# Optimization experiments

Hardware: AMD Instinct MI355X
Metric: run time of the kernel (lower is better)

Reference implementation:

```python
import jax, jax.numpy as jnp
import numpy as np

N = 200000          # nodes
E = 12_800_000      # edges (avg degree 64)
C = 4               # conv_out_channels == node_features
H = 32              # lstm_out_channels


def setup_inputs() -> dict:
    key = jax.random.key(0)
    ks = jax.random.split(key, 16)
    inv_c = 1.0 / np.sqrt(C)
    inv_h = 1.0 / np.sqrt(H)
    return {
        "x": jax.random.normal(ks[0], (N, C), jnp.float32),
        "edge_index": jax.random.randint(ks[1], (2, E), 0, N, dtype=jnp.int64),
        "edge_weight": jax.random.uniform(ks[2], (E,), jnp.float32),
        "h_0": 0.1 * jax.random.normal(ks[3], (1, N, H), jnp.float32),
        "c_0": 0.1 * jax.random.normal(ks[4], (1, N, H), jnp.float32),
        # GatedGraphConv (num_layers=1): weight[0] of shape [C, C]
        "conv_weight": inv_c * jax.random.normal(ks[5], (C, C), jnp.float32),
        # GRUCell(C, C) params (PyTorch layout: [3C, C], gate order r,z,n)
        "gru_w_ih": inv_c * jax.random.normal(ks[6], (3 * C, C), jnp.float32),
        "gru_w_hh": inv_c * jax.random.normal(ks[7], (3 * C, C), jnp.float32),
        "gru_b_ih": inv_c * jax.random.normal(ks[8], (3 * C,), jnp.float32),
        "gru_b_hh": inv_c * jax.random.normal(ks[9], (3 * C,), jnp.float32),
        # LSTM(C, H, 1 layer) params (PyTorch layout: [4H, *], gate order i,f,g,o)
        "lstm_w_ih": inv_h * jax.random.normal(ks[10], (4 * H, C), jnp.float32),
        "lstm_w_hh": inv_h * jax.random.normal(ks[11], (4 * H, H), jnp.float32),
        "lstm_b_ih": inv_h * jax.random.normal(ks[12], (4 * H,), jnp.float32),
        "lstm_b_hh": inv_h * jax.random.normal(ks[13], (4 * H,), jnp.float32),
        # Linear(32, 1)
        "lin_w": inv_h * jax.random.normal(ks[14], (1, H), jnp.float32),
        "lin_b": inv_h * jax.random.normal(ks[15], (1,), jnp.float32),
    }


def reference(x, edge_index, edge_weight, h_0, c_0,
              conv_weight, gru_w_ih, gru_w_hh, gru_b_ih, gru_b_hh,
              lstm_w_ih, lstm_w_hh, lstm_b_ih, lstm_b_hh, lin_w, lin_b):
    n = x.shape[0]
    src, dst = edge_index[0], edge_index[1]  # source j -> target i

    # ---- GatedGraphConv, 1 layer (in_dim == out_channels, no padding) ----
    m = x @ conv_weight                                   # [N, C]
    msg = m[src] * edge_weight[:, None]                   # [E, C] gather
    summed = jax.ops.segment_sum(msg, dst, num_segments=n)
    cnt = jax.ops.segment_sum(jnp.ones((msg.shape[0],), msg.dtype), dst,
                              num_segments=n)
    agg = summed / jnp.maximum(cnt, 1.0)[:, None]         # mean aggr (empty -> 0)

    # GRUCell(agg, x): r,z,n gate order
    gi = agg @ gru_w_ih.T + gru_b_ih
    gh = x @ gru_w_hh.T + gru_b_hh
    i_r, i_z, i_n = jnp.split(gi, 3, axis=1)
    h_r, h_z, h_n = jnp.split(gh, 3, axis=1)
    r = jax.nn.sigmoid(i_r + h_r)
    z = jax.nn.sigmoid(i_z + h_z)
    nn_ = jnp.tanh(i_n + r * h_n)
    h_conv = (1.0 - z) * nn_ + z * x                      # [N, C]

    # ---- LSTM: seq_len=1, batch=N, 1 layer; gate order i,f,g,o ----
    h_prev, c_prev = h_0[0], c_0[0]                       # [N, H]
    gates = h_conv @ lstm_w_ih.T + lstm_b_ih + h_prev @ lstm_w_hh.T + lstm_b_hh
    ig, fg, gg, og = jnp.split(gates, 4, axis=1)
    ig, fg, og = jax.nn.sigmoid(ig), jax.nn.sigmoid(fg), jax.nn.sigmoid(og)
    gg = jnp.tanh(gg)
    c_new = fg * c_prev + ig * gg
    h_new = og * jnp.tanh(c_new)                          # [N, H]

    # ---- relu + linear head ----
    out = jax.nn.relu(h_new) @ lin_w.T + lin_b            # [N, 1]
    return out, h_new[None], c_new[None]
```

## Files before the change

### kernel.cpp

```cpp
#include <hip/hip_runtime.h>
#include <math.h>

#define B_SHIFT 8
#define BMASK   255
#define CHUNK   16384
#define NTHR    256

static __device__ __forceinline__ float sigf(float x) {
  return 1.0f / (1.0f + __expf(-x));
}
static __device__ __forceinline__ float tanhfast(float x) {
  return 2.0f / (1.0f + __expf(-2.0f * x)) - 1.0f;
}

__global__ void conv_m_kernel(const float* __restrict__ x,
                              const float* __restrict__ w,
                              float* __restrict__ m, int n) {
  int i = blockIdx.x * blockDim.x + threadIdx.x;
  if (i >= n) return;
  float4 xv = reinterpret_cast<const float4*>(x)[i];
  float4 mv;
  mv.x = xv.x * w[0] + xv.y * w[4] + xv.z * w[8]  + xv.w * w[12];
  mv.y = xv.x * w[1] + xv.y * w[5] + xv.z * w[9]  + xv.w * w[13];
  mv.z = xv.x * w[2] + xv.y * w[6] + xv.z * w[10] + xv.w * w[14];
  mv.w = xv.x * w[3] + xv.y * w[7] + xv.z * w[11] + xv.w * w[15];
  reinterpret_cast<float4*>(m)[i] = mv;
}


__global__ __launch_bounds__(NTHR) void hist_kernel(const int* __restrict__ dst,
                                                    int E, int B,
                                                    int* __restrict__ gCnt) {
  __shared__ int h[1024];
  for (int b = threadIdx.x; b < B; b += NTHR) h[b] = 0;
  __syncthreads();
  const int4* d4 = reinterpret_cast<const int4*>(dst);
  int i4base = (int)(((long long)blockIdx.x * CHUNK) >> 2);
  int lim4 = E >> 2;
#pragma unroll
  for (int j = 0; j < 16; ++j) {
    int i4 = i4base + j * NTHR + threadIdx.x;
    if (i4 < lim4) {
      int4 d = d4[i4];
      atomicAdd(&h[d.x >> B_SHIFT], 1);
      atomicAdd(&h[d.y >> B_SHIFT], 1);
      atomicAdd(&h[d.z >> B_SHIFT], 1);
      atomicAdd(&h[d.w >> B_SHIFT], 1);
    }
  }
  if (blockIdx.x == 0 && threadIdx.x == 0) {
    for (int e = E & ~3; e < E; ++e) atomicAdd(&h[dst[e] >> B_SHIFT], 1);
  }
  __syncthreads();
  for (int b = threadIdx.x; b < B; b += NTHR) {
    int c = h[b];
    if (c) atomicAdd(&gCnt[b], c);
  }
}

__global__ void scan_kernel(const int* __restrict__ gCnt, int B,
                            int* __restrict__ start, int* __restrict__ cursor) {
  __shared__ int s[1024];
  int t = threadIdx.x;
  int v = (t < B) ? gCnt[t] : 0;
  s[t] = v;
  __syncthreads();
  for (int off = 1; off < 1024; off <<= 1) {
    int u = (t >= off) ? s[t - off] : 0;
    __syncthreads();
    s[t] += u;
    __syncthreads();
  }
  if (t < B) {
    int excl = (t == 0) ? 0 : s[t - 1];
    start[t] = excl;
    cursor[t] = excl;
  }
  if (t == 0) start[B] = s[1023];
}

__global__ __launch_bounds__(NTHR) void bin_kernel(const int* __restrict__ ei,
                                                   const float* __restrict__ ew,
                                                   int E, int B,
                                                   int* __restrict__ cursor,
                                                   int2* __restrict__ binned) {
  __shared__ int h[1024];
  for (int b = threadIdx.x; b < B; b += NTHR) h[b] = 0;
  __syncthreads();
  const int* dst = ei + E;
  const int4* d4 = reinterpret_cast<const int4*>(dst);
  const int4* s4 = reinterpret_cast<const int4*>(ei);
  const float4* w4 = reinterpret_cast<const float4*>(ew);
  int i4base = (int)(((long long)blockIdx.x * CHUNK) >> 2);
  int lim4 = E >> 2;
#pragma unroll
  for (int j = 0; j < 16; ++j) {
    int i4 = i4base + j * NTHR + threadIdx.x;
    if (i4 < lim4) {
      int4 d = d4[i4];
      atomicAdd(&h[d.x >> B_SHIFT], 1);
      atomicAdd(&h[d.y >> B_SHIFT], 1);
      atomicAdd(&h[d.z >> B_SHIFT], 1);
      atomicAdd(&h[d.w >> B_SHIFT], 1);
    }
  }
  __syncthreads();
  for (int b = threadIdx.x; b < B; b += NTHR) {
    int c = h[b];
    if (c) h[b] = atomicAdd(&cursor[b], c);
  }
  __syncthreads();
#pragma unroll
  for (int j = 0; j < 16; ++j) {
    int i4 = i4base + j * NTHR + threadIdx.x;
    if (i4 < lim4) {
      int4 d = d4[i4];
      int4 s = s4[i4];
      float4 w = w4[i4];
      int p;
      p = atomicAdd(&h[d.x >> B_SHIFT], 1);
      binned[p] = make_int2((s.x << B_SHIFT) | (d.x & BMASK), __float_as_int(w.x));
      p = atomicAdd(&h[d.y >> B_SHIFT], 1);
      binned[p] = make_int2((s.y << B_SHIFT) | (d.y & BMASK), __float_as_int(w.y));
      p = atomicAdd(&h[d.z >> B_SHIFT], 1);
      binned[p] = make_int2((s.z << B_SHIFT) | (d.z & BMASK), __float_as_int(w.z));
      p = atomicAdd(&h[d.w >> B_SHIFT], 1);
      binned[p] = make_int2((s.w << B_SHIFT) | (d.w & BMASK), __float_as_int(w.w));
    }
  }
  if (blockIdx.x == 0 && threadIdx.x == 0) {
    for (int e = E & ~3; e < E; ++e) {
      int d = dst[e];
      int p = atomicAdd(&cursor[d >> B_SHIFT], 1);
      binned[p] = make_int2((ei[e] << B_SHIFT) | (d & BMASK), __float_as_int(ew[e]));
    }
  }
}

__global__ __launch_bounds__(NTHR) void agg_node_kernel(
    const float* __restrict__ x, const float* __restrict__ m,
    const int2* __restrict__ binned, const int* __restrict__ start,
    const float* __restrict__ h0, const float* __restrict__ c0,
    const float* __restrict__ gwi, const float* __restrict__ gwh,
    const float* __restrict__ gbi, const float* __restrict__ gbh,
    const float* __restrict__ lwi, const float* __restrict__ lwh,
    const float* __restrict__ lbi, const float* __restrict__ lbh,
    const float* __restrict__ linw, const float* __restrict__ linb,
    float* __restrict__ out, float* __restrict__ hout, float* __restrict__ cout,
    int n) {
  __shared__ float acc[NTHR * 5];
  int tid = threadIdx.x;
  for (int idx = tid; idx < NTHR * 5; idx += NTHR) acc[idx] = 0.0f;
  __syncthreads();

  int s = start[blockIdx.x], e = start[blockIdx.x + 1];
  const float4* m4 = reinterpret_cast<const float4*>(m);
  for (int i = s + tid; i < e; i += NTHR) {
    int2 r = binned[i];
    int src = r.x >> B_SHIFT;
    int dl = r.x & BMASK;
    float w = __int_as_float(r.y);
    float4 mv = m4[src];
    atomicAdd(&acc[dl * 5 + 0], mv.x * w);
    atomicAdd(&acc[dl * 5 + 1], mv.y * w);
    atomicAdd(&acc[dl * 5 + 2], mv.z * w);
    atomicAdd(&acc[dl * 5 + 3], mv.w * w);
    atomicAdd(&acc[dl * 5 + 4], 1.0f);
  }
  __syncthreads();

  int i = (blockIdx.x << B_SHIFT) + tid;
  if (i >= n) return;

  float inv = 1.0f / fmaxf(acc[tid * 5 + 4], 1.0f);
  float agg[4] = {acc[tid * 5 + 0] * inv, acc[tid * 5 + 1] * inv,
                  acc[tid * 5 + 2] * inv, acc[tid * 5 + 3] * inv};
  float4 xv = reinterpret_cast<const float4*>(x)[i];
  float xa[4] = {xv.x, xv.y, xv.z, xv.w};

  float hc[4];
#pragma unroll
  for (int c = 0; c < 4; ++c) {
    float gi_r = gbi[c],     gh_r = gbh[c];
    float gi_z = gbi[4 + c], gh_z = gbh[4 + c];
    float gi_n = gbi[8 + c], gh_n = gbh[8 + c];
#pragma unroll
    for (int k = 0; k < 4; ++k) {
      gi_r += agg[k] * gwi[c * 4 + k];       gh_r += xa[k] * gwh[c * 4 + k];
      gi_z += agg[k] * gwi[(4 + c) * 4 + k]; gh_z += xa[k] * gwh[(4 + c) * 4 + k];
      gi_n += agg[k] * gwi[(8 + c) * 4 + k]; gh_n += xa[k] * gwh[(8 + c) * 4 + k];
    }
    float r = sigf(gi_r + gh_r);
    float z = sigf(gi_z + gh_z);
    float nn = tanhfast(gi_n + r * gh_n);
    hc[c] = (1.0f - z) * nn + z * xa[c];
  }

  const float4* h04 = reinterpret_cast<const float4*>(h0) + (size_t)i * 8;
  const float4* c04 = reinterpret_cast<const float4*>(c0) + (size_t)i * 8;
  float hp[32];
#pragma unroll
  for (int q = 0; q < 8; ++q) {
    float4 hv = h04[q];
    hp[q * 4 + 0] = hv.x; hp[q * 4 + 1] = hv.y;
    hp[q * 4 + 2] = hv.z; hp[q * 4 + 3] = hv.w;
  }
  const float4* wih4 = reinterpret_cast<const float4*>(lwi);
  const float4* whh4 = reinterpret_cast<const float4*>(lwh);
  float oacc = linb[0];
  float4* hout4 = reinterpret_cast<float4*>(hout) + (size_t)i * 8;
  float4* cout4 = reinterpret_cast<float4*>(cout) + (size_t)i * 8;

#pragma unroll
  for (int jc = 0; jc < 8; ++jc) {
    float4 cpv = c04[jc];
    float cpa[4] = {cpv.x, cpv.y, cpv.z, cpv.w};
    float hn[4], cn[4];
#pragma unroll
    for (int jj = 0; jj < 4; ++jj) {
      int j = jc * 4 + jj;
      float gI = lbi[j]      + lbh[j];
      float gF = lbi[32 + j] + lbh[32 + j];
      float gG = lbi[64 + j] + lbh[64 + j];
      float gO = lbi[96 + j] + lbh[96 + j];
      float4 wi = wih4[j], wf = wih4[32 + j], wg = wih4[64 + j], wo = wih4[96 + j];
      gI += hc[0] * wi.x + hc[1] * wi.y + hc[2] * wi.z + hc[3] * wi.w;
      gF += hc[0] * wf.x + hc[1] * wf.y + hc[2] * wf.z + hc[3] * wf.w;
      gG += hc[0] * wg.x + hc[1] * wg.y + hc[2] * wg.z + hc[3] * wg.w;
      gO += hc[0] * wo.x + hc[1] * wo.y + hc[2] * wo.z + hc[3] * wo.w;
#pragma unroll
      for (int q = 0; q < 8; ++q) {
        float4 a = whh4[j * 8 + q];
        float4 b = whh4[(32 + j) * 8 + q];
        float4 g = whh4[(64 + j) * 8 + q];
        float4 o = whh4[(96 + j) * 8 + q];
        float p0 = hp[q * 4 + 0], p1 = hp[q * 4 + 1];
        float p2 = hp[q * 4 + 2], p3 = hp[q * 4 + 3];
        gI += p0 * a.x + p1 * a.y + p2 * a.z + p3 * a.w;
        gF += p0 * b.x + p1 * b.y + p2 * b.z + p3 * b.w;
        gG += p0 * g.x + p1 * g.y + p2 * g.z + p3 * g.w;
        gO += p0 * o.x + p1 * o.y + p2 * o.z + p3 * o.w;
      }
      float ig = sigf(gI), fg = sigf(gF), og = sigf(gO), gg = tanhfast(gG);
      float cnew = fg * cpa[jj] + ig * gg;
      float hnew = og * tanhfast(cnew);
      cn[jj] = cnew; hn[jj] = hnew;
      oacc += fmaxf(hnew, 0.0f) * linw[j];
    }
    hout4[jc] = make_float4(hn[0], hn[1], hn[2], hn[3]);
    cout4[jc] = make_float4(cn[0], cn[1], cn[2], cn[3]);
  }
  out[i] = oacc;
}


__global__ void edge_kernel(const int* __restrict__ ei,
                            const float* __restrict__ ew,
                            const float* __restrict__ m,
                            float* __restrict__ summed,
                            float* __restrict__ cnt, int E) {
  int t = blockIdx.x * blockDim.x + threadIdx.x;
  int e0 = t * 4;
  const float4* m4 = reinterpret_cast<const float4*>(m);
  for (int e = e0; e < E && e < e0 + 4; ++e) {
    int s = ei[e], d = ei[E + e];
    float w = ew[e];
    float4 mv = m4[s];
    float* p = summed + 4ll * d;
    unsafeAtomicAdd(p + 0, mv.x * w);
    unsafeAtomicAdd(p + 1, mv.y * w);
    unsafeAtomicAdd(p + 2, mv.z * w);
    unsafeAtomicAdd(p + 3, mv.w * w);
    unsafeAtomicAdd(cnt + d, 1.0f);
  }
}

__global__ __launch_bounds__(NTHR) void node_kernel(
    const float* __restrict__ x, const float* __restrict__ summed,
    const float* __restrict__ cnt,
    const float* __restrict__ h0, const float* __restrict__ c0,
    const float* __restrict__ gwi, const float* __restrict__ gwh,
    const float* __restrict__ gbi, const float* __restrict__ gbh,
    const float* __restrict__ lwi, const float* __restrict__ lwh,
    const float* __restrict__ lbi, const float* __restrict__ lbh,
    const float* __restrict__ linw, const float* __restrict__ linb,
    float* __restrict__ out, float* __restrict__ hout, float* __restrict__ cout,
    int n) {
  int i = blockIdx.x * blockDim.x + threadIdx.x;
  if (i >= n) return;
  float4 sv = reinterpret_cast<const float4*>(summed)[i];
  float inv = 1.0f / fmaxf(cnt[i], 1.0f);
  float agg[4] = {sv.x * inv, sv.y * inv, sv.z * inv, sv.w * inv};
  float4 xv = reinterpret_cast<const float4*>(x)[i];
  float xa[4] = {xv.x, xv.y, xv.z, xv.w};
  float hc[4];
#pragma unroll
  for (int c = 0; c < 4; ++c) {
    float gi_r = gbi[c],     gh_r = gbh[c];
    float gi_z = gbi[4 + c], gh_z = gbh[4 + c];
    float gi_n = gbi[8 + c], gh_n = gbh[8 + c];
#pragma unroll
    for (int k = 0; k < 4; ++k) {
      gi_r += agg[k] * gwi[c * 4 + k];       gh_r += xa[k] * gwh[c * 4 + k];
      gi_z += agg[k] * gwi[(4 + c) * 4 + k]; gh_z += xa[k] * gwh[(4 + c) * 4 + k];
      gi_n += agg[k] * gwi[(8 + c) * 4 + k]; gh_n += xa[k] * gwh[(8 + c) * 4 + k];
    }
    float r = sigf(gi_r + gh_r);
    float z = sigf(gi_z + gh_z);
    float nn = tanhfast(gi_n + r * gh_n);
    hc[c] = (1.0f - z) * nn + z * xa[c];
  }
  const float4* h04 = reinterpret_cast<const float4*>(h0) + (size_t)i * 8;
  const float4* c04 = reinterpret_cast<const float4*>(c0) + (size_t)i * 8;
  float hp[32];
#pragma unroll
  for (int q = 0; q < 8; ++q) {
    float4 hv = h04[q];
    hp[q * 4 + 0] = hv.x; hp[q * 4 + 1] = hv.y;
    hp[q * 4 + 2] = hv.z; hp[q * 4 + 3] = hv.w;
  }
  const float4* wih4 = reinterpret_cast<const float4*>(lwi);
  const float4* whh4 = reinterpret_cast<const float4*>(lwh);
  float oacc = linb[0];
  float4* hout4 = reinterpret_cast<float4*>(hout) + (size_t)i * 8;
  float4* cout4 = reinterpret_cast<float4*>(cout) + (size_t)i * 8;
#pragma unroll
  for (int jc = 0; jc < 8; ++jc) {
    float4 cpv = c04[jc];
    float cpa[4] = {cpv.x, cpv.y, cpv.z, cpv.w};
    float hn[4], cn[4];
#pragma unroll
    for (int jj = 0; jj < 4; ++jj) {
      int j = jc * 4 + jj;
      float gI = lbi[j]      + lbh[j];
      float gF = lbi[32 + j] + lbh[32 + j];
      float gG = lbi[64 + j] + lbh[64 + j];
      float gO = lbi[96 + j] + lbh[96 + j];
      float4 wi = wih4[j], wf = wih4[32 + j], wg = wih4[64 + j], wo = wih4[96 + j];
      gI += hc[0] * wi.x + hc[1] * wi.y + hc[2] * wi.z + hc[3] * wi.w;
      gF += hc[0] * wf.x + hc[1] * wf.y + hc[2] * wf.z + hc[3] * wf.w;
      gG += hc[0] * wg.x + hc[1] * wg.y + hc[2] * wg.z + hc[3] * wg.w;
      gO += hc[0] * wo.x + hc[1] * wo.y + hc[2] * wo.z + hc[3] * wo.w;
#pragma unroll
      for (int q = 0; q < 8; ++q) {
        float4 a = whh4[j * 8 + q];
        float4 b = whh4[(32 + j) * 8 + q];
        float4 g = whh4[(64 + j) * 8 + q];
        float4 o = whh4[(96 + j) * 8 + q];
        float p0 = hp[q * 4 + 0], p1 = hp[q * 4 + 1];
        float p2 = hp[q * 4 + 2], p3 = hp[q * 4 + 3];
        gI += p0 * a.x + p1 * a.y + p2 * a.z + p3 * a.w;
        gF += p0 * b.x + p1 * b.y + p2 * b.z + p3 * b.w;
        gG += p0 * g.x + p1 * g.y + p2 * g.z + p3 * g.w;
        gO += p0 * o.x + p1 * o.y + p2 * o.z + p3 * o.w;
      }
      float ig = sigf(gI), fg = sigf(gF), og = sigf(gO), gg = tanhfast(gG);
      float cnew = fg * cpa[jj] + ig * gg;
      float hnew = og * tanhfast(cnew);
      cn[jj] = cnew; hn[jj] = hnew;
      oacc += fmaxf(hnew, 0.0f) * linw[j];
    }
    hout4[jc] = make_float4(hn[0], hn[1], hn[2], hn[3]);
    cout4[jc] = make_float4(cn[0], cn[1], cn[2], cn[3]);
  }
  out[i] = oacc;
}

extern "C" void kernel_launch(void* const* d_in, const int* in_sizes, int n_in,
                              void* d_out, int out_size, void* d_ws, size_t ws_size,
                              hipStream_t stream) {
  const float* x     = (const float*)d_in[0];
  const int*   ei    = (const int*)d_in[1];
  const float* ew    = (const float*)d_in[2];
  const float* h0    = (const float*)d_in[3];
  const float* c0    = (const float*)d_in[4];
  const float* convw = (const float*)d_in[5];
  const float* gwi   = (const float*)d_in[6];
  const float* gwh   = (const float*)d_in[7];
  const float* gbi   = (const float*)d_in[8];
  const float* gbh   = (const float*)d_in[9];
  const float* lwi   = (const float*)d_in[10];
  const float* lwh   = (const float*)d_in[11];
  const float* lbi   = (const float*)d_in[12];
  const float* lbh   = (const float*)d_in[13];
  const float* linw  = (const float*)d_in[14];
  const float* linb  = (const float*)d_in[15];

  int n = in_sizes[0] / 4;
  int E = in_sizes[1] / 2;

  float* out  = (float*)d_out;
  float* hout = out + n;
  float* cout = hout + (size_t)n * 32;

  int B = (n + BMASK) >> B_SHIFT;
  size_t need = (size_t)E * 8 + (size_t)n * 16 + ((size_t)3 * B + 2) * 4 + 64;

  if (B <= 1024 && ws_size >= need) {
    int2*  binned = (int2*)d_ws;
    float* m      = (float*)(binned + E);
    int*   gCnt   = (int*)(m + (size_t)n * 4);
    int*   start  = gCnt + B;
    int*   cursor = start + B + 1;

    hipMemsetAsync(gCnt, 0, (size_t)B * sizeof(int), stream);
    conv_m_kernel<<<(n + NTHR - 1) / NTHR, NTHR, 0, stream>>>(x, convw, m, n);

    int nbBlocks = (E + CHUNK - 1) / CHUNK;
    hist_kernel<<<nbBlocks, NTHR, 0, stream>>>(ei + E, E, B, gCnt);
    scan_kernel<<<1, 1024, 0, stream>>>(gCnt, B, start, cursor);
    bin_kernel<<<nbBlocks, NTHR, 0, stream>>>(ei, ew, E, B, cursor, binned);

    agg_node_kernel<<<B, NTHR, 0, stream>>>(
        x, m, binned, start, h0, c0,
        gwi, gwh, gbi, gbh, lwi, lwh, lbi, lbh, linw, linb,
        out, hout, cout, n);
  } else {
    float* m      = (float*)d_ws;
    float* summed = m + (size_t)n * 4;
    float* cntp   = summed + (size_t)n * 4;
    hipMemsetAsync(summed, 0, (size_t)n * 5 * sizeof(float), stream);
    conv_m_kernel<<<(n + NTHR - 1) / NTHR, NTHR, 0, stream>>>(x, convw, m, n);
    int et = (E + 3) / 4;
    edge_kernel<<<(et + NTHR - 1) / NTHR, NTHR, 0, stream>>>(ei, ew, m, summed, cntp, E);
    node_kernel<<<(n + NTHR - 1) / NTHR, NTHR, 0, stream>>>(
        x, summed, cntp, h0, c0,
        gwi, gwh, gbi, gbh, lwi, lwh, lbi, lbh, linw, linb,
        out, hout, cout, n);
  }
}
```

Before: 1.174 ms.

## Split fused aggregate+node kernel into separate aggregation and node kernels

Splits the fused per-bin aggregation and GRU/LSTM node kernel in two. A 512-thread agg_kernel gathers edges with 4-way unrolled nontemporal loads and writes summed and count arrays to workspace, and the existing node_kernel then runs the dense per-node math. The aim is to separate the latency-bound gather phase from the register-heavy LSTM phase so each runs at better occupancy. In exchange it adds an extra global round trip for the summed and count values (about 20 bytes per node) and one more kernel launch.

After: 1.183 ms. Within noise of the previous version (+0.8%).

```diff
diff --git a/kernel.cpp b/kernel.cpp
--- a/kernel.cpp
+++ b/kernel.cpp
@@ -5,6 +5,14 @@
 #define BMASK   255
 #define CHUNK   16384
 #define NTHR    256
+#define AGG_THR 512
+
+typedef int   v2i __attribute__((ext_vector_type(2)));
+typedef float v4f __attribute__((ext_vector_type(4)));
+
+static __device__ __forceinline__ v2i nt_load2i(const int2* p) {
+  return __builtin_nontemporal_load((const v2i*)p);
+}
 
 static __device__ __forceinline__ float sigf(float x) {
   return 1.0f / (1.0f + __expf(-x));
@@ -76,7 +84,7 @@
     start[t] = excl;
     cursor[t] = excl;
   }
-  if (t == 0) start[B] = s[1023];
+  if (t >= B && t < B + 8) start[t] = s[1023];
 }
 
 __global__ __launch_bounds__(NTHR) void bin_kernel(const int* __restrict__ ei,
@@ -137,30 +145,44 @@
   }
 }
 
-__global__ __launch_bounds__(NTHR) void agg_node_kernel(
-    const float* __restrict__ x, const float* __restrict__ m,
+__global__ __launch_bounds__(AGG_THR) void agg_kernel(
+    const float* __restrict__ m,
     const int2* __restrict__ binned, const int* __restrict__ start,
-    const float* __restrict__ h0, const float* __restrict__ c0,
-    const float* __restrict__ gwi, const float* __restrict__ gwh,
-    const float* __restrict__ gbi, const float* __restrict__ gbh,
-    const float* __restrict__ lwi, const float* __restrict__ lwh,
-    const float* __restrict__ lbi, const float* __restrict__ lbh,
-    const float* __restrict__ linw, const float* __restrict__ linb,
-    float* __restrict__ out, float* __restrict__ hout, float* __restrict__ cout,
-    int n) {
-  __shared__ float acc[NTHR * 5];
+    float* __restrict__ summed, float* __restrict__ cnt, int n) {
+  __shared__ float acc[256 * 5];
   int tid = threadIdx.x;
-  for (int idx = tid; idx < NTHR * 5; idx += NTHR) acc[idx] = 0.0f;
+  for (int idx = tid; idx < 256 * 5; idx += AGG_THR) acc[idx] = 0.0f;
   __syncthreads();
 
   int s = start[blockIdx.x], e = start[blockIdx.x + 1];
+  int len = e - s;
   const float4* m4 = reinterpret_cast<const float4*>(m);
-  for (int i = s + tid; i < e; i += NTHR) {
-    int2 r = binned[i];
-    int src = r.x >> B_SHIFT;
-    int dl = r.x & BMASK;
-    float w = __int_as_float(r.y);
-    float4 mv = m4[src];
+
+  int nFull = len >> 11;
+  for (int it = 0; it < nFull; ++it) {
+    int base = s + (it << 11) + (tid << 2);
+    v2i r[4];
+#pragma unroll
+    for (int k = 0; k < 4; ++k) r[k] = nt_load2i(binned + base + k);
+    float4 mv[4];
+#pragma unroll
+    for (int k = 0; k < 4; ++k) mv[k] = m4[r[k][0] >> B_SHIFT];
+#pragma unroll
+    for (int k = 0; k < 4; ++k) {
+      int dl = r[k][0] & BMASK;
+      float w = __int_as_float(r[k][1]);
+      atomicAdd(&acc[dl * 5 + 0], mv[k].x * w);
+      atomicAdd(&acc[dl * 5 + 1], mv[k].y * w);
+      atomicAdd(&acc[dl * 5 + 2], mv[k].z * w);
+      atomicAdd(&acc[dl * 5 + 3], mv[k].w * w);
+      atomicAdd(&acc[dl * 5 + 4], 1.0f);
+    }
+  }
+  for (int p = s + (nFull << 11) + tid; p < e; p += AGG_THR) {
+    v2i r = nt_load2i(binned + p);
+    int dl = r[0] & BMASK;
+    float w = __int_as_float(r[1]);
+    float4 mv = m4[r[0] >> B_SHIFT];
     atomicAdd(&acc[dl * 5 + 0], mv.x * w);
     atomicAdd(&acc[dl * 5 + 1], mv.y * w);
     atomicAdd(&acc[dl * 5 + 2], mv.z * w);
@@ -169,109 +191,14 @@
   }
   __syncthreads();
 
-  int i = (blockIdx.x << B_SHIFT) + tid;
-  if (i >= n) return;
-
-  float inv = 1.0f / fmaxf(acc[tid * 5 + 4], 1.0f);
-  float agg[4] = {acc[tid * 5 + 0] * inv, acc[tid * 5 + 1] * inv,
-                  acc[tid * 5 + 2] * inv, acc[tid * 5 + 3] * inv};
-  float4 xv = reinterpret_cast<const float4*>(x)[i];
-  float xa[4] = {xv.x, xv.y, xv.z, xv.w};
-
-  float hc[4];
-#pragma unroll
-  for (int c = 0; c < 4; ++c) {
-    float gi_r = gbi[c],     gh_r = gbh[c];
-    float gi_z = gbi[4 + c], gh_z = gbh[4 + c];
-    float gi_n = gbi[8 + c], gh_n = gbh[8 + c];
-#pragma unroll
-    for (int k = 0; k < 4; ++k) {
-      gi_r += agg[k] * gwi[c * 4 + k];       gh_r += xa[k] * gwh[c * 4 + k];
-      gi_z += agg[k] * gwi[(4 + c) * 4 + k]; gh_z += xa[k] * gwh[(4 + c) * 4 + k];
-      gi_n += agg[k] * gwi[(8 + c) * 4 + k]; gh_n += xa[k] * gwh[(8 + c) * 4 + k];
-    }
-    float r = sigf(gi_r + gh_r);
-    float z = sigf(gi_z + gh_z);
-    float nn = tanhfast(gi_n + r * gh_n);
-    hc[c] = (1.0f - z) * nn + z * xa[c];
-  }
-
-  const float4* h04 = reinterpret_cast<const float4*>(h0) + (size_t)i * 8;
-  const float4* c04 = reinterpret_cast<const float4*>(c0) + (size_t)i * 8;
-  float hp[32];
-#pragma unroll
-  for (int q = 0; q < 8; ++q) {
-    float4 hv = h04[q];
-    hp[q * 4 + 0] = hv.x; hp[q * 4 + 1] = hv.y;
-    hp[q * 4 + 2] = hv.z; hp[q * 4 + 3] = hv.w;
-  }
-  const float4* wih4 = reinterpret_cast<const float4*>(lwi);
-  const float4* whh4 = reinterpret_cast<const float4*>(lwh);
-  float oacc = linb[0];
-  float4* hout4 = reinterpret_cast<float4*>(hout) + (size_t)i * 8;
-  float4* cout4 = reinterpret_cast<float4*>(cout) + (size_t)i * 8;
-
-#pragma unroll
-  for (int jc = 0; jc < 8; ++jc) {
-    float4 cpv = c04[jc];
-    float cpa[4] = {cpv.x, cpv.y, cpv.z, cpv.w};
-    float hn[4], cn[4];
-#pragma unroll
-    for (int jj = 0; jj < 4; ++jj) {
-      int j = jc * 4 + jj;
-      float gI = lbi[j]      + lbh[j];
-      float gF = lbi[32 + j] + lbh[32 + j];
-      float gG = lbi[64 + j] + lbh[64 + j];
-      float gO = lbi[96 + j] + lbh[96 + j];
-      float4 wi = wih4[j], wf = wih4[32 + j], wg = wih4[64 + j], wo = wih4[96 + j];
-      gI += hc[0] * wi.x + hc[1] * wi.y + hc[2] * wi.z + hc[3] * wi.w;
-      gF += hc[0] * wf.x + hc[1] * wf.y + hc[2] * wf.z + hc[3] * wf.w;
-      gG += hc[0] * wg.x + hc[1] * wg.y + hc[2] * wg.z + hc[3] * wg.w;
-      gO += hc[0] * wo.x + hc[1] * wo.y + hc[2] * wo.z + hc[3] * wo.w;
-#pragma unroll
-      for (int q = 0; q < 8; ++q) {
-        float4 a = whh4[j * 8 + q];
-        float4 b = whh4[(32 + j) * 8 + q];
-        float4 g = whh4[(64 + j) * 8 + q];
-        float4 o = whh4[(96 + j) * 8 + q];
-        float p0 = hp[q * 4 + 0], p1 = hp[q * 4 + 1];
-        float p2 = hp[q * 4 + 2], p3 = hp[q * 4 + 3];
-        gI += p0 * a.x + p1 * a.y + p2 * a.z + p3 * a.w;
-        gF += p0 * b.x + p1 * b.y + p2 * b.z + p3 * b.w;
-        gG += p0 * g.x + p1 * g.y + p2 * g.z + p3 * g.w;
-        gO += p0 * o.x + p1 * o.y + p2 * o.z + p3 * o.w;
-      }
-      float ig = sigf(gI), fg = sigf(gF), og = sigf(gO), gg = tanhfast(gG);
-      float cnew = fg * cpa[jj] + ig * gg;
-      float hnew = og * tanhfast(cnew);
-      cn[jj] = cnew; hn[jj] = hnew;
-      oacc += fmaxf(hnew, 0.0f) * linw[j];
-    }
-    hout4[jc] = make_float4(hn[0], hn[1], hn[2], hn[3]);
-    cout4[jc] = make_float4(cn[0], cn[1], cn[2], cn[3]);
-  }
-  out[i] = oacc;
-}
-
-
-__global__ void edge_kernel(const int* __restrict__ ei,
-                            const float* __restrict__ ew,
-                            const float* __restrict__ m,
-                            float* __restrict__ summed,
-                            float* __restrict__ cnt, int E) {
-  int t = blockIdx.x * blockDim.x + threadIdx.x;
-  int e0 = t * 4;
-  const float4* m4 = reinterpret_cast<const float4*>(m);
-  for (int e = e0; e < E && e < e0 + 4; ++e) {
-    int s = ei[e], d = ei[E + e];
-    float w = ew[e];
-    float4 mv = m4[s];
-    float* p = summed + 4ll * d;
-    unsafeAtomicAdd(p + 0, mv.x * w);
-    unsafeAtomicAdd(p + 1, mv.y * w);
-    unsafeAtomicAdd(p + 2, mv.z * w);
-    unsafeAtomicAdd(p + 3, mv.w * w);
-    unsafeAtomicAdd(cnt + d, 1.0f);
+  if (tid < 256) {
+    int i = (blockIdx.x << B_SHIFT) + tid;
+    if (i < n) {
+      reinterpret_cast<float4*>(summed)[i] =
+          make_float4(acc[tid * 5 + 0], acc[tid * 5 + 1],
+                      acc[tid * 5 + 2], acc[tid * 5 + 3]);
+      cnt[i] = acc[tid * 5 + 4];
+    }
   }
 }
 
@@ -366,6 +293,28 @@
   out[i] = oacc;
 }
 
+
+__global__ void edge_kernel(const int* __restrict__ ei,
+                            const float* __restrict__ ew,
+                            const float* __restrict__ m,
+                            float* __restrict__ summed,
+                            float* __restrict__ cnt, int E) {
+  int t = blockIdx.x * blockDim.x + threadIdx.x;
+  int e0 = t * 4;
+  const float4* m4 = reinterpret_cast<const float4*>(m);
+  for (int e = e0; e < E && e < e0 + 4; ++e) {
+    int s = ei[e], d = ei[E + e];
+    float w = ew[e];
+    float4 mv = m4[s];
+    float* p = summed + 4ll * d;
+    unsafeAtomicAdd(p + 0, mv.x * w);
+    unsafeAtomicAdd(p + 1, mv.y * w);
+    unsafeAtomicAdd(p + 2, mv.z * w);
+    unsafeAtomicAdd(p + 3, mv.w * w);
+    unsafeAtomicAdd(cnt + d, 1.0f);
+  }
+}
+
 extern "C" void kernel_launch(void* const* d_in, const int* in_sizes, int n_in,
                               void* d_out, int out_size, void* d_ws, size_t ws_size,
                               hipStream_t stream) {
@@ -394,14 +343,18 @@
   float* cout = hout + (size_t)n * 32;
 
   int B = (n + BMASK) >> B_SHIFT;
-  size_t need = (size_t)E * 8 + (size_t)n * 16 + ((size_t)3 * B + 2) * 4 + 64;
-
-  if (B <= 1024 && ws_size >= need) {
+  size_t need = (size_t)E * 8 + (size_t)n * 16
+              + (size_t)n * 20
+              + ((size_t)3 * B + 16) * 4 + 64;
+
+  if (B <= 1016 && ws_size >= need) {
     int2*  binned = (int2*)d_ws;
     float* m      = (float*)(binned + E);
-    int*   gCnt   = (int*)(m + (size_t)n * 4);
+    float* summed = m + (size_t)n * 4;
+    float* cntp   = summed + (size_t)n * 4;
+    int*   gCnt   = (int*)(cntp + n);
     int*   start  = gCnt + B;
-    int*   cursor = start + B + 1;
+    int*   cursor = start + B + 8;
 
     hipMemsetAsync(gCnt, 0, (size_t)B * sizeof(int), stream);
     conv_m_kernel<<<(n + NTHR - 1) / NTHR, NTHR, 0, stream>>>(x, convw, m, n);
@@ -411,8 +364,10 @@
     scan_kernel<<<1, 1024, 0, stream>>>(gCnt, B, start, cursor);
     bin_kernel<<<nbBlocks, NTHR, 0, stream>>>(ei, ew, E, B, cursor, binned);
 
-    agg_node_kernel<<<B, NTHR, 0, stream>>>(
-        x, m, binned, start, h0, c0,
+    agg_kernel<<<B, AGG_THR, 0, stream>>>(m, binned, start, summed, cntp, n);
+
+    node_kernel<<<(n + NTHR - 1) / NTHR, NTHR, 0, stream>>>(
+        x, summed, cntp, h0, c0,
         gwi, gwh, gbi, gbh, lwi, lwh, lbi, lbh, linw, linb,
         out, hout, cout, n);
   } else {
```
